# Kernel optimization log

Measured on AMD Instinct MI355X. Metric: run time of the kernel, lower is better.

## Reference

```python
import jax, jax.numpy as jnp
import numpy as np

S, TM1, B, V, E, H = 96, 96, 8, 32000, 256, 512
PAD = 0
NEG = -1e30


def setup_inputs() -> dict:
    key = jax.random.key(0)
    ks = jax.random.split(key, 10)
    n = lambda k, shape, s=0.05: (jax.random.normal(k, shape, jnp.float32) * s)
    return {
        "src": jax.random.randint(ks[0], (S, B), 0, V, jnp.int32),
        "tgt": jax.random.randint(ks[1], (TM1 + 1, B), 0, V, jnp.int32),
        "emb": n(ks[2], (V, E)),
        "W_ih": n(ks[3], (4 * H, E)),
        "W_hh": n(ks[4], (4 * H, H)),
        "b_ih": jnp.zeros((4 * H,), jnp.float32),
        "b_hh": jnp.zeros((4 * H,), jnp.float32),
        "W_att": n(ks[5], (H, H)),
        "sent": n(ks[6], (H,)),
        "W_read": n(ks[7], (V, H)),
    }


def _lstm_cell(x, h, c, W_ih, W_hh, b_ih, b_hh):
    g = x @ W_ih.T + b_ih + h @ W_hh.T + b_hh
    i, f, gg, o = jnp.split(g, 4, axis=-1)
    c = jax.nn.sigmoid(f) * c + jax.nn.sigmoid(i) * jnp.tanh(gg)
    h = jax.nn.sigmoid(o) * jnp.tanh(c)
    return h, c


def _forward(src, tgt, emb, W_ih, W_hh, b_ih, b_hh, W_att, sent, W_read):
    # padding_idx behavior: pad row of embedding is zero (and gets no grad)
    emb_eff = emb * (jnp.arange(V) != PAD).astype(emb.dtype)[:, None]
    xs = jnp.concatenate([emb_eff[src], emb_eff[tgt[:-1]]], axis=0)  # [S+TM1,B,E]

    def step(carry, x):
        h, c = carry
        h, c = _lstm_cell(x, h, c, W_ih, W_hh, b_ih, b_hh)
        return (h, c), h

    init = (jnp.zeros((B, H), xs.dtype), jnp.zeros((B, H), xs.dtype))
    _, H_all = jax.lax.scan(step, init, xs)  # [S+TM1,B,H]

    H_dec = H_all[S:]                              # [TM1,B,H]
    Q = jnp.tanh(H_dec @ W_att.T)                  # [TM1,B,H]
    Z = jnp.einsum("tbh,jbh->tjb", Q, H_all)      # [TM1,S+TM1,B]
    zs = jnp.einsum("tbh,h->tb", Q, sent)         # sentinel logit
    logits = jnp.concatenate([Z, zs[:, None, :]], axis=1)  # [TM1,S+TM1+1,B]

    j = jnp.arange(S + TM1 + 1)
    t = jnp.arange(TM1)
    valid = (j[None, :] < S + t[:, None] + 1) | (j[None, :] == S + TM1)
    logits = jnp.where(valid[:, :, None], logits, NEG)
    a = jax.nn.softmax(logits, axis=1)
    a_src, a_tgt, a_sent = a[:, :S], a[:, S:S + TM1], a[:, -1]

    # pointer distributions via scatter-add (avoids dense one-hot [S,B,V])
    b_idx = jnp.arange(B)[None, None, :]
    t_idx = jnp.arange(TM1)[:, None, None]
    p_ptr = jnp.zeros((TM1, B, V), a.dtype)
    p_ptr = p_ptr.at[t_idx, b_idx, src[None, :, :]].add(a_src)
    p_ptr = p_ptr.at[t_idx, b_idx, tgt[:-1][None, :, :]].add(a_tgt)

    p_vocab = jax.nn.softmax(H_dec @ W_read.T, axis=-1)  # [TM1,B,V]
    p = p_ptr + p_vocab * a_sent[:, :, None]
    ptr_scores = p_ptr + a_sent[:, :, None]

    mask = (tgt != PAD).astype(p.dtype)  # [TM1+1,B]
    gold = jnp.take_along_axis(jnp.log(p), tgt[1:][:, :, None], axis=2)[..., 0] * mask[1:]
    gold_ptr = jnp.take_along_axis(jnp.log(ptr_scores), tgt[1:][:, :, None], axis=2)[..., 0] * mask[1:]
    return gold.sum(0), gold_ptr.sum(0)  # ([B], [B])


def reference(src, tgt, emb, W_ih, W_hh, b_ih, b_hh, W_att, sent, W_read):
    return _forward(src, tgt, emb, W_ih, W_hh, b_ih, b_hh, W_att, sent, W_read)
```

## Files before the change

kernel.cpp:

```cpp
#include <hip/hip_runtime.h>
#include <math.h>

#define SS   96
#define TM   96
#define BB   8
#define VV   32000
#define EE   256
#define HH   512
#define NTOK (SS + TM)
#define G4   (4 * HH)
#define NEGF (-1e30f)
#define LBLK 16

#define NXIH  768
#define NCVTW 512
#define NCVTR 8000
#define NPREP (NXIH + NCVTW + NCVTR)

typedef __attribute__((ext_vector_type(8))) short short8;
typedef __attribute__((ext_vector_type(4))) float f32x4;
typedef __attribute__((ext_vector_type(4))) unsigned uint32x4;
typedef unsigned long long u64;

#define XIH_OFF   ((size_t)0)
#define XIH_SZ    ((size_t)NTOK * BB * G4)
#define HALL_OFF  (XIH_OFF + XIH_SZ)
#define HALL_SZ   ((size_t)NTOK * BB * HH)
#define Q_OFF     (HALL_OFF + HALL_SZ)
#define Q_SZ      ((size_t)TM * BB * HH)
#define PPTR_OFF  (Q_OFF + Q_SZ)
#define ASENT_OFF (PPTR_OFF + (size_t)(TM * BB))
#define SSUM_OFF  (ASENT_OFF + (size_t)(TM * BB))
#define LSTAR_OFF (SSUM_OFF + (size_t)(TM * BB))
#define FLAG_OFF  (LSTAR_OFF + (size_t)(TM * BB))
#define HBF_OFF   (FLAG_OFF + (size_t)1024)
#define HBF_SZF   ((size_t)2 * BB * HH / 2)
#define WHHBF_OFF (HBF_OFF + HBF_SZF)
#define WHHBF_SZF ((size_t)G4 * HH / 2)
#define ABF_OFF   (WHHBF_OFF + WHHBF_SZF)
#define ABF_SZF   ((size_t)(TM * BB) * HH / 2)
#define WBF_OFF   (ABF_OFF + ABF_SZF)
#define WBF_SZF   ((size_t)VV * HH / 2)
#define NEED_F    (WBF_OFF + WBF_SZF)

__device__ __forceinline__ float sigf(float x) { return 1.f / (1.f + __expf(-x)); }

__device__ __forceinline__ unsigned short f2bf(float x) {
    unsigned bits = __float_as_uint(x);
    bits += 0x7FFFu + ((bits >> 16) & 1u);
    return (unsigned short)(bits >> 16);
}

__global__ void __launch_bounds__(256) k_prep(const int* __restrict__ src,
                                              const int* __restrict__ tgt,
                                              const float* __restrict__ emb,
                                              const float* __restrict__ Wih,
                                              const float* __restrict__ bih,
                                              const float* __restrict__ bhh,
                                              const float* __restrict__ Whh,
                                              const float* __restrict__ Wread,
                                              float* __restrict__ xih,
                                              unsigned short* __restrict__ whhbf,
                                              unsigned short* __restrict__ wbf) {
    __shared__ float xs[16 * EE];
    const int bid = blockIdx.x;
    const int tid = threadIdx.x;

    if (bid < NXIH) {
        const int tok0 = (bid >> 3) * 16;
        const int row0 = (bid & 7) * 256;
        for (int e = tid; e < 16 * EE; e += 256) {
            int tk = e >> 8, k = e & 255;
            int tau = tok0 + tk;
            int idx = (tau < SS * BB) ? src[tau] : tgt[tau - SS * BB];
            xs[tk * EE + k] = (idx == 0) ? 0.f : emb[(size_t)idx * EE + k];
        }
        __syncthreads();

        const int row = row0 + tid;
        const float bias = bih[row] + bhh[row];
        float acc[16];
#pragma unroll
        for (int r = 0; r < 16; ++r) acc[r] = bias;
        const float4* w4 = (const float4*)(Wih + (size_t)row * EE);
        for (int k4 = 0; k4 < EE / 4; ++k4) {
            float4 w = w4[k4];
#pragma unroll
            for (int r = 0; r < 16; ++r) {
                float4 x = *((const float4*)&xs[r * EE + k4 * 4]);
                acc[r] += w.x * x.x + w.y * x.y + w.z * x.z + w.w * x.w;
            }
        }
#pragma unroll
        for (int r = 0; r < 16; ++r)
            xih[(size_t)(tok0 + r) * G4 + row] = acc[r];
        return;
    }

    const float* srcp;
    unsigned short* dstp;
    size_t base;
    if (bid < NXIH + NCVTW) { srcp = Whh;   dstp = whhbf; base = (size_t)(bid - NXIH) * 2048; }
    else                    { srcp = Wread; dstp = wbf;   base = (size_t)(bid - NXIH - NCVTW) * 2048; }
    base += (size_t)tid * 8;
    float4 f0 = *(const float4*)(srcp + base);
    float4 f1 = *(const float4*)(srcp + base + 4);
    uint4 o;
    o.x = (unsigned)f2bf(f0.x) | ((unsigned)f2bf(f0.y) << 16);
    o.y = (unsigned)f2bf(f0.z) | ((unsigned)f2bf(f0.w) << 16);
    o.z = (unsigned)f2bf(f1.x) | ((unsigned)f2bf(f1.y) << 16);
    o.w = (unsigned)f2bf(f1.z) | ((unsigned)f2bf(f1.w) << 16);
    *(uint4*)(dstp + base) = o;
}

__global__ void __launch_bounds__(256, 1) k_lstm(const float* __restrict__ xih,
                                                 const unsigned short* __restrict__ whhbf,
                                                 float* __restrict__ hall,
                                                 unsigned short* __restrict__ hbf,
                                                 unsigned short* __restrict__ abf,
                                                 unsigned* __restrict__ flags) {
    extern __shared__ short lA[];
    const int tid = threadIdx.x;
    const int wv  = tid >> 6;
    const int l   = tid & 63;
    const int b16 = l & 15;
    const int kg  = l >> 4;
    const int bb  = b16 & 7;
    const int bx  = blockIdx.x;
    const int I0  = bx * 32 + wv * 8;
    unsigned* myflag = flags + (size_t)(bx * 4 + wv) * 16;

    const int j = b16;
    const unsigned short* a0p = whhbf + ((size_t)((j >> 3) * HH + I0 + (j & 7))) * HH + kg * 8;
    const unsigned short* a1p = whhbf + ((size_t)((2 + (j >> 3)) * HH + I0 + (j & 7))) * HH + kg * 8;
    short* lA0 = lA + (((size_t)wv * 2 + 0) * 16 * 64 + l) * 8;
    short* lA1 = lA + (((size_t)wv * 2 + 1) * 16 * 64 + l) * 8;
#pragma unroll
    for (int ks = 0; ks < 16; ++ks) {
        *(short8*)(lA0 + ks * 512) = *(const short8*)(a0p + ks * 32);
        *(short8*)(lA1 + ks * 512) = *(const short8*)(a1p + ks * 32);
    }
    __syncthreads();

    const int xgate0 = (kg >> 1);
    const int xgate1 = 2 + (kg >> 1);
    const int xi     = I0 + (kg & 1) * 4;

    float c0[4] = {0.f, 0.f, 0.f, 0.f};
    union fragu { uint32x4 u4; short8 s; };

    for (int t = 0; t < NTOK; ++t) {
        const float* xb = xih + ((size_t)t * BB + bb) * G4;
        float4 x0 = *(const float4*)(xb + xgate0 * HH + xi);
        float4 x1 = *(const float4*)(xb + xgate1 * HH + xi);

        fragu Bf[16];
        if (t > 0) {
            while (__hip_atomic_load(&flags[(size_t)l * 16], __ATOMIC_RELAXED,
                                     __HIP_MEMORY_SCOPE_AGENT) < (unsigned)t) {}

            const unsigned short* hsrc =
                hbf + ((t - 1) & 1) * (BB * HH) + (size_t)bb * HH + kg * 8;
#pragma unroll
            for (int ks = 0; ks < 16; ++ks)
                asm volatile("global_load_dwordx4 %0, %1, off sc0 sc1"
                             : "=v"(Bf[ks].u4) : "v"(hsrc + ks * 32) : "memory");
            asm volatile("s_waitcnt vmcnt(0)" ::: "memory");
            __builtin_amdgcn_sched_barrier(0);
        }

        f32x4 acc0 = {x0.x, x0.y, x0.z, x0.w};
        f32x4 acc1 = {x1.x, x1.y, x1.z, x1.w};
        if (t > 0) {
#pragma unroll
            for (int ks = 0; ks < 16; ++ks) {
                short8 a0 = *(const short8*)(lA0 + ks * 512);
                short8 a1 = *(const short8*)(lA1 + ks * 512);
                acc0 = __builtin_amdgcn_mfma_f32_16x16x32_bf16(a0, Bf[ks].s, acc0, 0, 0, 0);
                acc1 = __builtin_amdgcn_mfma_f32_16x16x32_bf16(a1, Bf[ks].s, acc1, 0, 0, 0);
            }
        }

        float hreg[4];
#pragma unroll
        for (int r = 0; r < 4; ++r) {
            float gf = __shfl_down(acc0[r], 32, 64);
            float go = __shfl_down(acc1[r], 32, 64);
            float is = sigf(acc0[r]);
            float fs = sigf(gf);
            float gv = tanhf(acc1[r]);
            float os = sigf(go);
            c0[r] = fs * c0[r] + is * gv;
            hreg[r] = os * tanhf(c0[r]);
        }

        if (l < 32 && b16 < BB) {
            const int ib = I0 + kg * 4;
            *(float4*)(hall + ((size_t)t * BB + b16) * HH + ib) =
                make_float4(hreg[0], hreg[1], hreg[2], hreg[3]);
            u64 pk = (u64)f2bf(hreg[0]) | ((u64)f2bf(hreg[1]) << 16) |
                     ((u64)f2bf(hreg[2]) << 32) | ((u64)f2bf(hreg[3]) << 48);
            if (t >= SS)
                *(u64*)(abf + ((size_t)(t - SS) * BB + b16) * HH + ib) = pk;
            if (t < NTOK - 1) {
                unsigned short* hdst = hbf + (t & 1) * (BB * HH) + (size_t)b16 * HH + ib;
                asm volatile("global_store_dwordx2 %0, %1, off sc0 sc1"
                             :: "v"(hdst), "v"(pk) : "memory");
            }
        }

        if (t < NTOK - 1) {
            asm volatile("s_waitcnt vmcnt(0)" ::: "memory");
            if (l == 0)
                __hip_atomic_store(myflag, (unsigned)(t + 1),
                                   __ATOMIC_RELAXED, __HIP_MEMORY_SCOPE_AGENT);
        }
    }
}

__global__ void __launch_bounds__(256) k_q(const float* __restrict__ hall,
                                           const float* __restrict__ Watt,
                                           float* __restrict__ q) {
    __shared__ float hb[8 * 516];
    const int t = blockIdx.x, tid = threadIdx.x;
    const float* hdec = hall + (size_t)(SS + t) * (BB * HH);
    for (int e = tid; e < BB * HH; e += 256)
        hb[(e >> 9) * 516 + (e & 511)] = hdec[e];
    __syncthreads();

    for (int oi = tid; oi < BB * HH; oi += 256) {
        int b = oi & 7, ii = oi >> 3;
        const float4* w4 = (const float4*)(Watt + (size_t)ii * HH);
        const float4* h4 = (const float4*)(hb + b * 516);
        float acc = 0.f;
        for (int k4 = 0; k4 < HH / 4; ++k4) {
            float4 w = w4[k4], h = h4[k4];
            acc += w.x * h.x + w.y * h.y + w.z * h.z + w.w * h.w;
        }
        q[(size_t)(t * BB + b) * HH + ii] = tanhf(acc);
    }
}

__global__ void __launch_bounds__(256) k_att(const float* __restrict__ hall,
                                             const float* __restrict__ q,
                                             const float* __restrict__ sent,
                                             const int* __restrict__ src,
                                             const int* __restrict__ tgt,
                                             float* __restrict__ pptr,
                                             float* __restrict__ asent) {
    __shared__ float qs[HH];
    __shared__ float av[256];
    __shared__ float red[256];
    const int t = blockIdx.x, b = blockIdx.y, tid = threadIdx.x;

    for (int e = tid; e < HH; e += 256) qs[e] = q[(size_t)(t * BB + b) * HH + e];
    __syncthreads();

    const int j = tid;
    float acc = NEGF;
    if (j < SS + TM + 1) {
        bool valid = (j < SS + t + 1) || (j == SS + TM);
        if (valid) {
            const float* vptr = (j < SS + TM) ? (hall + (size_t)(j * BB + b) * HH) : sent;
            const float4* v4 = (const float4*)vptr;
            const float4* q4 = (const float4*)qs;
            float a = 0.f;
            for (int k4 = 0; k4 < HH / 4; ++k4) {
                float4 v = v4[k4], qq = q4[k4];
                a += v.x * qq.x + v.y * qq.y + v.z * qq.z + v.w * qq.w;
            }
            acc = a;
        }
    }
    red[tid] = acc;
    __syncthreads();
    for (int s2 = 128; s2 > 0; s2 >>= 1) {
        if (tid < s2) red[tid] = fmaxf(red[tid], red[tid + s2]);
        __syncthreads();
    }
    float m = red[0];
    __syncthreads();
    float e = __expf(acc - m);
    red[tid] = e;
    __syncthreads();
    for (int s2 = 128; s2 > 0; s2 >>= 1) {
        if (tid < s2) red[tid] += red[tid + s2];
        __syncthreads();
    }
    float denom = red[0];
    __syncthreads();
    float a = e / denom;
    av[tid] = a;
    __syncthreads();

    const int vs = tgt[(t + 1) * BB + b];
    float contrib = 0.f;
    if (j < SS) {
        if (src[j * BB + b] == vs) contrib += av[j];
        if (tgt[j * BB + b] == vs) contrib += av[SS + j];
    }
    red[tid] = contrib;
    __syncthreads();
    for (int s2 = 128; s2 > 0; s2 >>= 1) {
        if (tid < s2) red[tid] += red[tid + s2];
        __syncthreads();
    }
    if (tid == 0) {
        pptr[t * BB + b]  = red[0];
        asent[t * BB + b] = av[SS + TM];
    }
}

__global__ void __launch_bounds__(256) k_vocab_mfma(const unsigned short* __restrict__ Abf,
                                                    const unsigned short* __restrict__ Wbf,
                                                    const int* __restrict__ tgt,
                                                    float* __restrict__ ssum,
                                                    float* __restrict__ lstar) {
    const int tid  = threadIdx.x;
    const int wave = tid >> 6;
    const int lane = tid & 63;
    const int r16  = lane & 15;
    const int kg   = lane >> 4;
    const int n0   = blockIdx.x * 64;

    const unsigned short* b0 = Wbf + (size_t)(n0 +  0 + r16) * HH + kg * 8;
    const unsigned short* b1 = Wbf + (size_t)(n0 + 16 + r16) * HH + kg * 8;
    const unsigned short* b2 = Wbf + (size_t)(n0 + 32 + r16) * HH + kg * 8;
    const unsigned short* b3 = Wbf + (size_t)(n0 + 48 + r16) * HH + kg * 8;

    for (int pass = 0; pass < 12; ++pass) {
        const int row0 = pass * 64 + wave * 16;
        const unsigned short* arow = Abf + (size_t)(row0 + r16) * HH + kg * 8;

        f32x4 acc0 = {0.f,0.f,0.f,0.f}, acc1 = acc0, acc2 = acc0, acc3 = acc0;
#pragma unroll
        for (int ks = 0; ks < 16; ++ks) {
            short8 a = *(const short8*)(arow + ks * 32);
            acc0 = __builtin_amdgcn_mfma_f32_16x16x32_bf16(a, *(const short8*)(b0 + ks * 32), acc0, 0, 0, 0);
            acc1 = __builtin_amdgcn_mfma_f32_16x16x32_bf16(a, *(const short8*)(b1 + ks * 32), acc1, 0, 0, 0);
            acc2 = __builtin_amdgcn_mfma_f32_16x16x32_bf16(a, *(const short8*)(b2 + ks * 32), acc2, 0, 0, 0);
            acc3 = __builtin_amdgcn_mfma_f32_16x16x32_bf16(a, *(const short8*)(b3 + ks * 32), acc3, 0, 0, 0);
        }

#pragma unroll
        for (int reg = 0; reg < 4; ++reg) {
            const int rowg = row0 + 4 * kg + reg;
            const int vs = tgt[BB + rowg];
            int cg;
            cg = n0 +  0 + r16; if (cg == vs) lstar[rowg] = acc0[reg];
            cg = n0 + 16 + r16; if (cg == vs) lstar[rowg] = acc1[reg];
            cg = n0 + 32 + r16; if (cg == vs) lstar[rowg] = acc2[reg];
            cg = n0 + 48 + r16; if (cg == vs) lstar[rowg] = acc3[reg];

            float v = __expf(acc0[reg]) + __expf(acc1[reg]) +
                      __expf(acc2[reg]) + __expf(acc3[reg]);
            v += __shfl_xor(v, 1, 64);
            v += __shfl_xor(v, 2, 64);
            v += __shfl_xor(v, 4, 64);
            v += __shfl_xor(v, 8, 64);
            if (r16 == 0) atomicAdd(&ssum[rowg], v);
        }
    }
}

__global__ void __launch_bounds__(256) k_vocab_f32(const float* __restrict__ hall,
                                                   const float* __restrict__ Wread,
                                                   const int* __restrict__ tgt,
                                                   float* __restrict__ ssum,
                                                   float* __restrict__ lstar) {
    __shared__ float hs[32 * HH];
    const int tid = threadIdx.x;
    const int v0 = blockIdx.x * 512 + tid * 2;
    const int v1 = v0 + 1;
    const bool g0 = v0 < VV, g1 = v1 < VV;
    const float4* w40 = (const float4*)(Wread + (size_t)(g0 ? v0 : 0) * HH);
    const float4* w41 = (const float4*)(Wread + (size_t)(g1 ? v1 : 0) * HH);
    const int rbase0 = blockIdx.y * 128;

    for (int ch = 0; ch < 4; ++ch) {
        const int rbase = rbase0 + ch * 32;
        const float4* sp4 = (const float4*)(hall + ((size_t)SS * BB + rbase) * HH);
        float4* hs4 = (float4*)hs;
        for (int e = tid; e < 32 * HH / 4; e += 256) hs4[e] = sp4[e];
        __syncthreads();

        float acc0[32], acc1[32];
#pragma unroll
        for (int r = 0; r < 32; ++r) { acc0[r] = 0.f; acc1[r] = 0.f; }

        for (int k4 = 0; k4 < HH / 4; ++k4) {
            float4 w0 = w40[k4];
            float4 w1 = w41[k4];
#pragma unroll
            for (int r = 0; r < 32; ++r) {
                float4 h = *((const float4*)(hs + r * HH + k4 * 4));
                acc0[r] += w0.x * h.x + w0.y * h.y + w0.z * h.z + w0.w * h.w;
                acc1[r] += w1.x * h.x + w1.y * h.y + w1.z * h.z + w1.w * h.w;
            }
        }

#pragma unroll
        for (int r = 0; r < 32; ++r) {
            const int row = rbase + r;
            float val = 0.f;
            if (g0) val += __expf(acc0[r]);
            if (g1) val += __expf(acc1[r]);
#pragma unroll
            for (int d = 32; d > 0; d >>= 1) val += __shfl_xor(val, d, 64);
            if ((tid & 63) == 0) atomicAdd(&ssum[row], val);
            const int vs = tgt[row + BB];
            if (g0 && v0 == vs) lstar[row] = acc0[r];
            else if (g1 && v1 == vs) lstar[row] = acc1[r];
        }
        __syncthreads();
    }
}

__global__ void __launch_bounds__(768) k_final(const float* __restrict__ pptr,
                                               const float* __restrict__ asent,
                                               const float* __restrict__ ssum,
                                               const float* __restrict__ lstar,
                                               const int* __restrict__ tgt,
                                               float* __restrict__ out) {
    __shared__ float g[TM * BB], gp[TM * BB];
    const int tid = threadIdx.x;
    const int vs = tgt[tid + BB];
    const float pv = __expf(lstar[tid]) / ssum[tid];
    const float ps = pptr[tid];
    const float as = asent[tid];
    if (vs != 0) {
        g[tid]  = logf(ps + pv * as);
        gp[tid] = logf(ps + as);
    } else {
        g[tid] = 0.f; gp[tid] = 0.f;
    }
    __syncthreads();
    if (tid < BB) {
        float s1 = 0.f, s2 = 0.f;
        for (int t = 0; t < TM; ++t) { s1 += g[t * BB + tid]; s2 += gp[t * BB + tid]; }
        out[tid] = s1;
        out[BB + tid] = s2;
    }
}

extern "C" void kernel_launch(void* const* d_in, const int* in_sizes, int n_in,
                              void* d_out, int out_size, void* d_ws, size_t ws_size,
                              hipStream_t stream) {
    (void)in_sizes; (void)n_in; (void)out_size;
    const int*   src   = (const int*)d_in[0];
    const int*   tgt   = (const int*)d_in[1];
    const float* emb   = (const float*)d_in[2];
    const float* Wih   = (const float*)d_in[3];
    const float* Whh   = (const float*)d_in[4];
    const float* bih   = (const float*)d_in[5];
    const float* bhh   = (const float*)d_in[6];
    const float* Watt  = (const float*)d_in[7];
    const float* sent  = (const float*)d_in[8];
    const float* Wread = (const float*)d_in[9];
    float* ws  = (float*)d_ws;
    float* out = (float*)d_out;

    const bool use_mfma_vocab = ws_size >= NEED_F * sizeof(float);

    (void)hipMemsetAsync((void*)(ws + SSUM_OFF), 0, (size_t)2560 * sizeof(float), stream);

    k_prep<<<dim3(NPREP), 256, 0, stream>>>(
        src, tgt, emb, Wih, bih, bhh, Whh, Wread,
        ws + XIH_OFF, (unsigned short*)(ws + WHHBF_OFF), (unsigned short*)(ws + WBF_OFF));

    {
        const float* xih = ws + XIH_OFF;
        const unsigned short* whhbf = (const unsigned short*)(ws + WHHBF_OFF);
        float* hall = ws + HALL_OFF;
        unsigned short* hbf = (unsigned short*)(ws + HBF_OFF);
        unsigned short* abf = (unsigned short*)(ws + ABF_OFF);
        unsigned* flags = (unsigned*)(ws + FLAG_OFF);
        void* args[] = { (void*)&xih, (void*)&whhbf, (void*)&hall,
                         (void*)&hbf, (void*)&abf, (void*)&flags };
        (void)hipLaunchCooperativeKernel((void*)k_lstm, dim3(LBLK), dim3(256), args,
                                         131072, stream);
    }

    k_q<<<dim3(TM), 256, 0, stream>>>(ws + HALL_OFF, Watt, ws + Q_OFF);

    k_att<<<dim3(TM, BB), 256, 0, stream>>>(ws + HALL_OFF, ws + Q_OFF, sent,
                                            src, tgt, ws + PPTR_OFF, ws + ASENT_OFF);

    if (use_mfma_vocab) {
        k_vocab_mfma<<<dim3(VV / 64), 256, 0, stream>>>(
            (const unsigned short*)(ws + ABF_OFF),
            (const unsigned short*)(ws + WBF_OFF),
            tgt, ws + SSUM_OFF, ws + LSTAR_OFF);
    } else {
        k_vocab_f32<<<dim3(63, 6), 256, 0, stream>>>(ws + HALL_OFF, Wread, tgt,
                                                     ws + SSUM_OFF, ws + LSTAR_OFF);
    }

    k_final<<<dim3(1), dim3(TM * BB), 0, stream>>>(ws + PPTR_OFF, ws + ASENT_OFF,
                                                   ws + SSUM_OFF, ws + LSTAR_OFF,
                                                   tgt, out);
}
```

Baseline: 1.420 ms.

## Use per-block flags in LSTM recurrence and stage vocab weights in LDS

```diff
diff --git a/kernel.cpp b/kernel.cpp
--- a/kernel.cpp
+++ b/kernel.cpp
@@ -119,7 +119,7 @@
                                                  unsigned short* __restrict__ hbf,
                                                  unsigned short* __restrict__ abf,
                                                  unsigned* __restrict__ flags) {
-    extern __shared__ short lA[];
+    __shared__ short lA[65536];
     const int tid = threadIdx.x;
     const int wv  = tid >> 6;
     const int l   = tid & 63;
@@ -128,7 +128,6 @@
     const int bb  = b16 & 7;
     const int bx  = blockIdx.x;
     const int I0  = bx * 32 + wv * 8;
-    unsigned* myflag = flags + (size_t)(bx * 4 + wv) * 16;
 
     const int j = b16;
     const unsigned short* a0p = whhbf + ((size_t)((j >> 3) * HH + I0 + (j & 7))) * HH + kg * 8;
@@ -156,9 +155,10 @@
 
         fragu Bf[16];
         if (t > 0) {
-            while (__hip_atomic_load(&flags[(size_t)l * 16], __ATOMIC_RELAXED,
-                                     __HIP_MEMORY_SCOPE_AGENT) < (unsigned)t) {}
-
+            if (l < 16) {
+                while (__hip_atomic_load(&flags[(size_t)l * 16], __ATOMIC_RELAXED,
+                                         __HIP_MEMORY_SCOPE_AGENT) < (unsigned)t) {}
+            }
             const unsigned short* hsrc =
                 hbf + ((t - 1) & 1) * (BB * HH) + (size_t)bb * HH + kg * 8;
 #pragma unroll
@@ -211,8 +211,9 @@
 
         if (t < NTOK - 1) {
             asm volatile("s_waitcnt vmcnt(0)" ::: "memory");
-            if (l == 0)
-                __hip_atomic_store(myflag, (unsigned)(t + 1),
+            __syncthreads();
+            if (tid == 0)
+                __hip_atomic_store(&flags[(size_t)bx * 16], (unsigned)(t + 1),
                                    __ATOMIC_RELAXED, __HIP_MEMORY_SCOPE_AGENT);
         }
     }
@@ -316,30 +317,37 @@
                                                     const int* __restrict__ tgt,
                                                     float* __restrict__ ssum,
                                                     float* __restrict__ lstar) {
+    __shared__ short lB[32768];
     const int tid  = threadIdx.x;
-    const int wave = tid >> 6;
     const int lane = tid & 63;
     const int r16  = lane & 15;
     const int kg   = lane >> 4;
     const int n0   = blockIdx.x * 64;
 
-    const unsigned short* b0 = Wbf + (size_t)(n0 +  0 + r16) * HH + kg * 8;
-    const unsigned short* b1 = Wbf + (size_t)(n0 + 16 + r16) * HH + kg * 8;
-    const unsigned short* b2 = Wbf + (size_t)(n0 + 32 + r16) * HH + kg * 8;
-    const unsigned short* b3 = Wbf + (size_t)(n0 + 48 + r16) * HH + kg * 8;
+    for (int s = tid; s < 4096; s += 256) {
+        const int slot = s >> 6;
+        const int cb = slot >> 4, ks = slot & 15;
+        const int ll = s & 63;
+        const int rr = ll & 15, kk = ll >> 4;
+        *(short8*)(lB + (size_t)s * 8) =
+            *(const short8*)(Wbf + (size_t)(n0 + cb * 16 + rr) * HH + ks * 32 + kk * 8);
+    }
+    __syncthreads();
+
+    const short* lBme = lB + (size_t)lane * 8;
 
     for (int pass = 0; pass < 12; ++pass) {
-        const int row0 = pass * 64 + wave * 16;
+        const int row0 = pass * 64 + (tid >> 6) * 16;
         const unsigned short* arow = Abf + (size_t)(row0 + r16) * HH + kg * 8;
 
         f32x4 acc0 = {0.f,0.f,0.f,0.f}, acc1 = acc0, acc2 = acc0, acc3 = acc0;
 #pragma unroll
         for (int ks = 0; ks < 16; ++ks) {
             short8 a = *(const short8*)(arow + ks * 32);
-            acc0 = __builtin_amdgcn_mfma_f32_16x16x32_bf16(a, *(const short8*)(b0 + ks * 32), acc0, 0, 0, 0);
-            acc1 = __builtin_amdgcn_mfma_f32_16x16x32_bf16(a, *(const short8*)(b1 + ks * 32), acc1, 0, 0, 0);
-            acc2 = __builtin_amdgcn_mfma_f32_16x16x32_bf16(a, *(const short8*)(b2 + ks * 32), acc2, 0, 0, 0);
-            acc3 = __builtin_amdgcn_mfma_f32_16x16x32_bf16(a, *(const short8*)(b3 + ks * 32), acc3, 0, 0, 0);
+            acc0 = __builtin_amdgcn_mfma_f32_16x16x32_bf16(a, *(const short8*)(lBme + (size_t)(0 * 16 + ks) * 512), acc0, 0, 0, 0);
+            acc1 = __builtin_amdgcn_mfma_f32_16x16x32_bf16(a, *(const short8*)(lBme + (size_t)(1 * 16 + ks) * 512), acc1, 0, 0, 0);
+            acc2 = __builtin_amdgcn_mfma_f32_16x16x32_bf16(a, *(const short8*)(lBme + (size_t)(2 * 16 + ks) * 512), acc2, 0, 0, 0);
+            acc3 = __builtin_amdgcn_mfma_f32_16x16x32_bf16(a, *(const short8*)(lBme + (size_t)(3 * 16 + ks) * 512), acc3, 0, 0, 0);
         }
 
 #pragma unroll
@@ -468,18 +476,10 @@
         src, tgt, emb, Wih, bih, bhh, Whh, Wread,
         ws + XIH_OFF, (unsigned short*)(ws + WHHBF_OFF), (unsigned short*)(ws + WBF_OFF));
 
-    {
-        const float* xih = ws + XIH_OFF;
-        const unsigned short* whhbf = (const unsigned short*)(ws + WHHBF_OFF);
-        float* hall = ws + HALL_OFF;
-        unsigned short* hbf = (unsigned short*)(ws + HBF_OFF);
-        unsigned short* abf = (unsigned short*)(ws + ABF_OFF);
-        unsigned* flags = (unsigned*)(ws + FLAG_OFF);
-        void* args[] = { (void*)&xih, (void*)&whhbf, (void*)&hall,
-                         (void*)&hbf, (void*)&abf, (void*)&flags };
-        (void)hipLaunchCooperativeKernel((void*)k_lstm, dim3(LBLK), dim3(256), args,
-                                         131072, stream);
-    }
+    k_lstm<<<dim3(LBLK), 256, 0, stream>>>(
+        ws + XIH_OFF, (const unsigned short*)(ws + WHHBF_OFF), ws + HALL_OFF,
+        (unsigned short*)(ws + HBF_OFF), (unsigned short*)(ws + ABF_OFF),
+        (unsigned*)(ws + FLAG_OFF));
 
     k_q<<<dim3(TM), 256, 0, stream>>>(ws + HALL_OFF, Watt, ws + Q_OFF);
 
```

New measurement: 1.293 ms. -8.9%, faster.
